# Optimization experiments

Hardware: AMD Instinct MI355X
Metric: run time of the kernel (lower is better)

The kernel has to match this reference:

```python
import jax, jax.numpy as jnp
import numpy as np

B, E, C, H = 128, 512, 128, 8
D = E // H
K = 21  # kNN neighbors per electrode (min(21, C))


def setup_inputs() -> dict:
    key = jax.random.key(0)
    ks = jax.random.split(key, 7)
    x = jax.random.normal(ks[0], (B, E, C), dtype=jnp.float32)
    # 1x1 Conv1d with no bias == [E_out, E_in] matmul over the feature dim
    wq = jax.random.normal(ks[1], (E, E), dtype=jnp.float32) * (E ** -0.5)
    wk = jax.random.normal(ks[2], (E, E), dtype=jnp.float32) * (E ** -0.5)
    wv = jax.random.normal(ks[3], (E, E), dtype=jnp.float32) * (E ** -0.5)
    wo = jax.random.normal(ks[4], (E, E), dtype=jnp.float32) * (E ** -0.5)
    dir_vec = jax.random.normal(ks[5], (H, C), dtype=jnp.float32)

    # synthetic electrode positions (stands in for electrode_positions.pt)
    pos = jax.random.normal(ks[6], (C, 3), dtype=jnp.float32)

    # arc_dist: great-circle distance scaled by mean radius
    radii = jnp.linalg.norm(pos, axis=1, keepdims=True)
    posn = pos / radii
    dist = jnp.arccos(jnp.clip(posn @ posn.T, -1.0, 1.0)) * radii.mean()

    # Gaussian spatial bias, row-mean centered
    sigma = jnp.median(jnp.tril(dist, 1))
    attn_bias = -dist ** 2 / (2.0 * sigma ** 2 + 1e-8)
    attn_bias = attn_bias - attn_bias.mean(axis=1, keepdims=True)

    # unit displacement vectors, zeroed on the diagonal: disp[i,j] = unit(pos[j]-pos[i])
    disp = pos[None, :, :] - pos[:, None, :]
    disp = disp / jnp.clip(jnp.linalg.norm(disp, axis=-1, keepdims=True), 1e-8)
    disp = disp.at[jnp.arange(C), jnp.arange(C)].set(0.0)

    # kNN mask: K smallest distances per row (includes self)
    _, knn_idx = jax.lax.top_k(-dist, K)
    knn_mask = jnp.zeros((C, C), dtype=bool).at[jnp.arange(C)[:, None], knn_idx].set(True)

    return {"x": x, "wq": wq, "wk": wk, "wv": wv, "wo": wo,
            "dir_vec": dir_vec, "attn_bias": attn_bias,
            "displacement": disp, "knn_mask": knn_mask}


def reference(x, wq, wk, wv, wo, dir_vec, attn_bias, displacement, knn_mask):
    scale = D ** -0.5
    # q/k/v projections: 1x1 conv (no bias) + SELU, then split heads -> [B,H,D,C]
    q = jax.nn.selu(jnp.einsum('oe,bec->boc', wq, x)).reshape(B, H, D, C)
    k = jax.nn.selu(jnp.einsum('oe,bec->boc', wk, x)).reshape(B, H, D, C)
    v = jax.nn.selu(jnp.einsum('oe,bec->boc', wv, x)).reshape(B, H, D, C)

    # scores[b,h,i,j] = <q[...,i], k[...,j]> * scale + spatial bias
    scores = jnp.einsum('bhdi,bhdj->bhij', q, k) * scale + attn_bias[None, None]

    # per-head antisymmetric directional bias
    dvn = dir_vec / jnp.clip(jnp.linalg.norm(dir_vec, axis=-1, keepdims=True), 1e-12)
    dir_bias = displacement.mean(axis=-1)[None, :, :] * dvn[:, None, :]  # [H,C,C]
    dir_bias = 0.5 * (dir_bias - jnp.swapaxes(dir_bias, -1, -2))
    scores = scores + (dir_bias - dir_bias.mean(axis=-1, keepdims=True))[None]

    # kNN masking + stable softmax
    scores = jnp.where(knn_mask[None, None], scores, -jnp.inf)
    scores = scores - scores.max(axis=-1, keepdims=True)
    p = jax.nn.softmax(scores, axis=-1)

    # aggregate values and merge heads -> [B, E, C]
    attn = jnp.einsum('bhij,bhdj->bhdi', p, v).reshape(B, E, C)
    # output projection (AlphaDropout is identity in eval)
    return jax.nn.selu(jnp.einsum('oe,bec->boc', wo, attn))
```

## Files before the change

### kernel.cpp

```cpp
#include <hip/hip_runtime.h>
#include <math.h>

#define B_ 128
#define E_ 512
#define C_ 128
#define H_ 8
#define D_ 64
#define BEC_ ((size_t)B_ * E_ * C_)

typedef __attribute__((ext_vector_type(8))) __bf16 bf16x8;
typedef __attribute__((ext_vector_type(4))) float f32x4;

__device__ __forceinline__ ushort f2bf(float f) {
    unsigned u = __float_as_uint(f);
    unsigned r = u + 0x7fffu + ((u >> 16) & 1u);
    return (ushort)(r >> 16);
}
__device__ __forceinline__ float bf2f(ushort h) {
    return __uint_as_float(((unsigned)h) << 16);
}
__device__ __forceinline__ void split_bf(float f, ushort& hi, ushort& lo) {
    hi = f2bf(f);
    lo = f2bf(f - bf2f(hi));
}
__device__ __forceinline__ float selu_f(float x) {
    const float alpha = 1.6732632423543772f;
    const float scale = 1.0507009873554805f;
    return x > 0.0f ? scale * x : scale * alpha * expm1f(x);
}
__device__ __forceinline__ void gll16(const void* g, void* l) {
    __builtin_amdgcn_global_load_lds(
        (const __attribute__((address_space(1))) void*)g,
        (__attribute__((address_space(3))) void*)l, 16, 0, 0);
}

__global__ void detect_mask_kernel(const unsigned char* __restrict__ m,
                                   int* __restrict__ flag) {
    __shared__ int cnt;
    if (threadIdx.x == 0) cnt = 0;
    __syncthreads();
    int local = 0;
    for (int i = threadIdx.x; i < C_ * C_; i += blockDim.x) local += (m[i] != 0);
    atomicAdd(&cnt, local);
    __syncthreads();
    if (threadIdx.x == 0) *flag = (cnt > 1600) ? 1 : 0;
}

__global__ __launch_bounds__(128) void bias_prep_kernel(
    const float* __restrict__ dir_vec, const float* __restrict__ attn_bias,
    const float* __restrict__ disp, const unsigned char* __restrict__ maskb,
    const int* __restrict__ flag, float* __restrict__ combT)
{
    const int i = blockIdx.x, h = blockIdx.y, j = threadIdx.x;
    __shared__ float red[128];

    float dv = dir_vec[h * C_ + j];
    red[j] = dv * dv;
    __syncthreads();
    for (int s = 64; s > 0; s >>= 1) {
        if (j < s) red[j] += red[j + s];
        __syncthreads();
    }
    const float nrm = fmaxf(sqrtf(red[0]), 1e-12f);
    __syncthreads();

    const float dvn_j = dir_vec[h * C_ + j] / nrm;
    const float dvn_i = dir_vec[h * C_ + i] / nrm;
    const float third = 1.0f / 3.0f;
    const float dm_ij = (disp[(i * C_ + j) * 3 + 0] + disp[(i * C_ + j) * 3 + 1] +
                         disp[(i * C_ + j) * 3 + 2]) * third;
    const float dm_ji = (disp[(j * C_ + i) * 3 + 0] + disp[(j * C_ + i) * 3 + 1] +
                         disp[(j * C_ + i) * 3 + 2]) * third;
    const float db = 0.5f * (dm_ij * dvn_j - dm_ji * dvn_i);

    red[j] = db;
    __syncthreads();
    for (int s = 64; s > 0; s >>= 1) {
        if (j < s) red[j] += red[j + s];
        __syncthreads();
    }
    const float rowmean = red[0] * (1.0f / 128.0f);

    const bool mk = (*flag) ? (maskb[i * C_ + j] != 0)
                            : (((const int*)maskb)[i * C_ + j] != 0);
    combT[((size_t)h * C_ + j) * C_ + i] =
        mk ? (attn_bias[i * C_ + j] + db - rowmean) : -INFINITY;
}

__global__ __launch_bounds__(256) void wsplit_kernel(
    const float* __restrict__ w0, const float* __restrict__ w1,
    const float* __restrict__ w2, const float* __restrict__ w3,
    ushort* __restrict__ wh, ushort* __restrict__ wl)
{
    const int s = blockIdx.y;
    const float* __restrict__ w = (s == 0) ? w0 : (s == 1) ? w1 : (s == 2) ? w2 : w3;
    const size_t base = (size_t)s * E_ * E_;
    const size_t i0 = ((size_t)blockIdx.x * 256 + threadIdx.x) * 8;
    const float4 f0 = *(const float4*)&w[i0];
    const float4 f1 = *(const float4*)&w[i0 + 4];
    const float ff[8] = {f0.x, f0.y, f0.z, f0.w, f1.x, f1.y, f1.z, f1.w};
    union { ushort u[8]; uint4 v; } hu, lu;
#pragma unroll
    for (int j = 0; j < 8; ++j) split_bf(ff[j], hu.u[j], lu.u[j]);
    *(uint4*)&wh[base + i0] = hu.v;
    *(uint4*)&wl[base + i0] = lu.v;
}

__global__ __launch_bounds__(256) void xsplit_kernel(
    const float* __restrict__ x, ushort* __restrict__ xh, ushort* __restrict__ xl)
{
    const int b = blockIdx.y, e0 = blockIdx.x * 64;
    __shared__ float ts[64][132];
    const int tid = threadIdx.x;
    const float* __restrict__ xb = x + ((size_t)b * E_ + e0) * C_;
#pragma unroll
    for (int r = 0; r < 8; ++r) {
        const int idx = tid + r * 256;
        const int e = idx >> 5, c4 = idx & 31;
        *(float4*)&ts[e][c4 * 4] = *(const float4*)&xb[(size_t)e * C_ + c4 * 4];
    }
    __syncthreads();
    const int lc = tid >> 3;
    const int l8 = (tid & 7) * 8;
#pragma unroll
    for (int p = 0; p < 4; ++p) {
        const int c = p * 32 + lc;
        union { ushort u[8]; uint4 v; } hu, lu;
#pragma unroll
        for (int j = 0; j < 8; ++j) split_bf(ts[l8 + j][c], hu.u[j], lu.u[j]);
        const size_t rb = ((size_t)b * C_ + c) * E_ + e0 + l8;
        *(uint4*)&xh[rb] = hu.v;
        *(uint4*)&xl[rb] = lu.v;
    }
}

template<int MODE>
__global__ __launch_bounds__(512, 1) void gemm8_kernel(
    const ushort* __restrict__ Wh, const ushort* __restrict__ Wl,
    const ushort* __restrict__ Bh, const ushort* __restrict__ Bl,
    ushort* __restrict__ qh, ushort* __restrict__ ql,
    ushort* __restrict__ kh, ushort* __restrict__ kl,
    ushort* __restrict__ vhp, float* __restrict__ fout)
{
    __shared__ ushort lds[3 * 24576];

    const int NB = (MODE == 0) ? 12 : 4;
    const int nwg = NB * 64;
    const int w = blockIdx.x + NB * blockIdx.y;
    const int l = (w & 7) * (nwg >> 3) + (w >> 3);
    const int bx = l % NB, bgrp = l / NB;

    const int tid = threadIdx.x, wid = tid >> 6, lane = tid & 63;
    const int o0 = bx * 128;
    const int wr = wid >> 2, wc = wid & 3, l15 = lane & 15;
    const int kq = (lane >> 4) * 16;

    const char* sp[6];
    size_t so[6];
    int lo_[6];
#pragma unroll
    for (int q = 0; q < 6; ++q) {
        const int g = wid * 6 + q;
        int stream, inst;
        if (g < 8)       { stream = 0; inst = g; }
        else if (g < 16) { stream = 1; inst = g - 8; }
        else if (g < 32) { stream = 2; inst = g - 16; }
        else             { stream = 3; inst = g - 32; }
        const int rowbase = (stream < 2) ? (o0 + inst * 16)
                                         : (bgrp * 256 + inst * 16);
        sp[q] = (stream == 0) ? (const char*)Wh : (stream == 1) ? (const char*)Wl
              : (stream == 2) ? (const char*)Bh : (const char*)Bl;
        so[q] = ((size_t)(rowbase + (lane >> 2)) * E_) * 2 + (size_t)(lane & 3) * 16;
        lo_[q] = ((stream == 0) ? 0 : (stream == 1) ? 4096 :
                  (stream == 2) ? 8192 : 16384) + inst * 512;
    }

    int aoff[4], boff[4];
#pragma unroll
    for (int m = 0; m < 4; ++m) aoff[m] = (wr * 64 + m * 16 + l15) * 64 + kq;
#pragma unroll
    for (int n = 0; n < 4; ++n) boff[n] = (wc * 64 + n * 16 + l15) * 64 + kq;

    f32x4 acc[4][4];
#pragma unroll
    for (int m = 0; m < 4; ++m)
#pragma unroll
        for (int n = 0; n < 4; ++n) acc[m][n] = (f32x4)0.0f;

#pragma unroll
    for (int p = 0; p < 3; ++p) {
#pragma unroll
        for (int q = 0; q < 6; ++q)
            gll16(sp[q] + so[q] + (size_t)p * 64, &lds[p * 24576 + lo_[q]]);
    }

    int cur = 0;
    for (int t = 0; t < 16; ++t) {
        const char* bb = (const char*)lds + cur * 49152;

        asm volatile("s_waitcnt vmcnt(12)" ::: "memory");
        __builtin_amdgcn_s_barrier();
        __builtin_amdgcn_sched_barrier(0);

        bf16x8 ah[4], al[4], bh4[4], bl4[4];
#pragma unroll
        for (int m = 0; m < 2; ++m) {
            ah[m] = *(const bf16x8*)(bb + aoff[m]);
            al[m] = *(const bf16x8*)(bb + 8192 + aoff[m]);
        }
#pragma unroll
        for (int n = 0; n < 4; ++n) {
            bh4[n] = *(const bf16x8*)(bb + 16384 + boff[n]);
            bl4[n] = *(const bf16x8*)(bb + 32768 + boff[n]);
        }
        __builtin_amdgcn_s_setprio(1);
#pragma unroll
        for (int m = 0; m < 2; ++m)
#pragma unroll
            for (int n = 0; n < 4; ++n) {
                acc[m][n] = __builtin_amdgcn_mfma_f32_16x16x32_bf16(
                    ah[m], bh4[n], acc[m][n], 0, 0, 0);
                acc[m][n] = __builtin_amdgcn_mfma_f32_16x16x32_bf16(
                    ah[m], bl4[n], acc[m][n], 0, 0, 0);
                acc[m][n] = __builtin_amdgcn_mfma_f32_16x16x32_bf16(
                    al[m], bh4[n], acc[m][n], 0, 0, 0);
            }
        __builtin_amdgcn_s_setprio(0);

#pragma unroll
        for (int m = 2; m < 4; ++m) {
            ah[m] = *(const bf16x8*)(bb + aoff[m]);
            al[m] = *(const bf16x8*)(bb + 8192 + aoff[m]);
        }
        asm volatile("s_waitcnt lgkmcnt(0)" ::: "memory");
        __builtin_amdgcn_sched_barrier(0);
        __builtin_amdgcn_s_barrier();

        {
            const int kt = (t + 3 > 15) ? 15 : t + 3;
#pragma unroll
            for (int q = 0; q < 6; ++q)
                gll16(sp[q] + so[q] + (size_t)kt * 64, &lds[cur * 24576 + lo_[q]]);
        }

        __builtin_amdgcn_s_setprio(1);
#pragma unroll
        for (int m = 2; m < 4; ++m)
#pragma unroll
            for (int n = 0; n < 4; ++n) {
                acc[m][n] = __builtin_amdgcn_mfma_f32_16x16x32_bf16(
                    ah[m], bh4[n], acc[m][n], 0, 0, 0);
                acc[m][n] = __builtin_amdgcn_mfma_f32_16x16x32_bf16(
                    ah[m], bl4[n], acc[m][n], 0, 0, 0);
                acc[m][n] = __builtin_amdgcn_mfma_f32_16x16x32_bf16(
                    al[m], bh4[n], acc[m][n], 0, 0, 0);
            }
        __builtin_amdgcn_s_setprio(0);

        cur = (cur == 2) ? 0 : cur + 1;
    }
    asm volatile("s_waitcnt vmcnt(0)" ::: "memory");

    const int lr4 = (lane >> 4) * 4;
    if (MODE == 1) {
        const int ob = bx * 128 + wr * 64;
#pragma unroll
        for (int m = 0; m < 4; ++m)
#pragma unroll
            for (int n = 0; n < 4; ++n) {
                const int R = bgrp * 256 + wc * 64 + n * 16 + l15;
                float* po = fout + ((size_t)(R >> 7) * E_ + ob + m * 16 + lr4) * C_ +
                            (R & 127);
                const f32x4 a = acc[m][n];
#pragma unroll
                for (int j = 0; j < 4; ++j) po[(size_t)j * C_] = selu_f(a[j]);
            }
    } else {
        const int z = bx >> 2;
        const int wo0 = (bx & 3) * 128 + wr * 64;
        if (z == 2) {
#pragma unroll
            for (int m = 0; m < 4; ++m)
#pragma unroll
                for (int n = 0; n < 4; ++n) {
                    const int R = bgrp * 256 + wc * 64 + n * 16 + l15;
                    const f32x4 a = acc[m][n];
#pragma unroll
                    for (int j = 0; j < 4; ++j)
                        vhp[((size_t)(R >> 7) * E_ + wo0 + m * 16 + lr4 + j) * C_ +
                            (R & 127)] = f2bf(selu_f(a[j]));
                }
        } else {
            ushort* __restrict__ th = z ? kh : qh;
            ushort* __restrict__ tl = z ? kl : ql;
#pragma unroll
            for (int m = 0; m < 4; ++m)
#pragma unroll
                for (int n = 0; n < 4; ++n) {
                    const int R = bgrp * 256 + wc * 64 + n * 16 + l15;
                    const int ol = wo0 + m * 16 + lr4;
                    union { ushort u[4]; uint2 v; } hu, lu;
                    const f32x4 a = acc[m][n];
#pragma unroll
                    for (int j = 0; j < 4; ++j) split_bf(selu_f(a[j]), hu.u[j], lu.u[j]);
                    *(uint2*)&th[(size_t)R * E_ + ol] = hu.v;
                    *(uint2*)&tl[(size_t)R * E_ + ol] = lu.v;
                }
        }
    }
}

__global__ __launch_bounds__(256, 2) void attn_mfma_kernel(
    const ushort* __restrict__ qTh, const ushort* __restrict__ qTl,
    const ushort* __restrict__ kTh, const ushort* __restrict__ kTl,
    const ushort* __restrict__ vh,  const float* __restrict__ combT,
    ushort* __restrict__ aTh, ushort* __restrict__ aTl)
{
    const int b = blockIdx.x, h = blockIdx.y;
    __shared__ ushort lds[40960];
    ushort* sQh = lds;
    ushort* sQl = lds + 8192;
    ushort* sKh = lds + 16384;
    ushort* sKl = lds + 24576;
    ushort* sV  = lds + 32768;
    ushort* sPh = lds;
    ushort* sPl = lds + 16384;

    const int tid = threadIdx.x, wid = tid >> 6, lane = tid & 63;

    {
        const size_t gq = (size_t)b * C_ * E_ + h * D_;
        const int rsub = lane >> 3, chunk = lane & 7;
#pragma unroll
        for (int t = 0; t < 4; ++t) {
            const int inst = wid * 4 + t;
            const int row = inst * 8 + rsub;
            const size_t goff = (gq + (size_t)row * E_) * 2 +
                                (size_t)(chunk ^ (row & 7)) * 16;
            gll16((const char*)qTh + goff, &sQh[inst * 512]);
            gll16((const char*)qTl + goff, &sQl[inst * 512]);
            gll16((const char*)kTh + goff, &sKh[inst * 512]);
            gll16((const char*)kTl + goff, &sKl[inst * 512]);
        }
        const size_t gv = ((size_t)b * E_ + h * D_) * C_;
        const int vr = lane >> 4, vchunk = lane & 15;
#pragma unroll
        for (int t = 0; t < 4; ++t) {
            const int inst = wid * 4 + t;
            const int row = inst * 4 + vr;
            const size_t goff = (gv + (size_t)row * C_) * 2 +
                                (size_t)(vchunk ^ (row & 7)) * 16;
            gll16((const char*)vh + goff, &sV[inst * 512]);
        }
    }
    __syncthreads();

    const int i0 = wid * 32;
    const int l15 = lane & 15;

    f32x4 acc[2][8];
#pragma unroll
    for (int m = 0; m < 2; ++m)
#pragma unroll
        for (int n = 0; n < 8; ++n) acc[m][n] = (f32x4)0.0f;

#pragma unroll
    for (int kk = 0; kk < 2; ++kk) {
        const int kbyte = kk * 64 + (lane >> 4) * 16;
        bf16x8 qhf[2], qlf[2];
#pragma unroll
        for (int m = 0; m < 2; ++m) {
            const int r = i0 + m * 16 + l15;
            const int byt = r * 128 + (kbyte ^ ((r & 7) << 4));
            qhf[m] = *(const bf16x8*)((const char*)sQh + byt);
            qlf[m] = *(const bf16x8*)((const char*)sQl + byt);
        }
#pragma unroll
        for (int n = 0; n < 8; ++n) {
            const int r = n * 16 + l15;
            const int byt = r * 128 + (kbyte ^ ((r & 7) << 4));
            const bf16x8 khf = *(const bf16x8*)((const char*)sKh + byt);
            const bf16x8 klf = *(const bf16x8*)((const char*)sKl + byt);
#pragma unroll
            for (int m = 0; m < 2; ++m) {
                acc[m][n] = __builtin_amdgcn_mfma_f32_16x16x32_bf16(
                    qhf[m], khf, acc[m][n], 0, 0, 0);
                acc[m][n] = __builtin_amdgcn_mfma_f32_16x16x32_bf16(
                    qhf[m], klf, acc[m][n], 0, 0, 0);
                acc[m][n] = __builtin_amdgcn_mfma_f32_16x16x32_bf16(
                    qlf[m], khf, acc[m][n], 0, 0, 0);
            }
        }
    }

#pragma unroll
    for (int m = 0; m < 2; ++m)
#pragma unroll
        for (int n = 0; n < 8; ++n) {
            const int jcol = n * 16 + l15;
            const float4 cb = *(const float4*)&combT[
                ((size_t)h * C_ + jcol) * C_ + i0 + m * 16 + (lane >> 4) * 4];
            acc[m][n][0] = fmaf(acc[m][n][0], 0.125f, cb.x);
            acc[m][n][1] = fmaf(acc[m][n][1], 0.125f, cb.y);
            acc[m][n][2] = fmaf(acc[m][n][2], 0.125f, cb.z);
            acc[m][n][3] = fmaf(acc[m][n][3], 0.125f, cb.w);
        }

#pragma unroll
    for (int m = 0; m < 2; ++m)
#pragma unroll
        for (int jj = 0; jj < 4; ++jj) {
            float mx = -INFINITY;
#pragma unroll
            for (int n = 0; n < 8; ++n) mx = fmaxf(mx, acc[m][n][jj]);
#pragma unroll
            for (int off = 1; off < 16; off <<= 1)
                mx = fmaxf(mx, __shfl_xor(mx, off));
            float sum = 0.0f;
#pragma unroll
            for (int n = 0; n < 8; ++n) {
                const float e = __expf(acc[m][n][jj] - mx);
                acc[m][n][jj] = e;
                sum += e;
            }
#pragma unroll
            for (int off = 1; off < 16; off <<= 1) sum += __shfl_xor(sum, off);
            const float inv = 1.0f / sum;
#pragma unroll
            for (int n = 0; n < 8; ++n) acc[m][n][jj] *= inv;
        }

    __syncthreads();
#pragma unroll
    for (int m = 0; m < 2; ++m)
#pragma unroll
        for (int n = 0; n < 8; ++n)
#pragma unroll
            for (int jj = 0; jj < 4; ++jj) {
                const int i = i0 + m * 16 + (lane >> 4) * 4 + jj;
                const int col = n * 16 + l15;
                const int byt = i * 256 + ((col * 2) ^ ((i & 7) << 4));
                ushort hi, lo;
                split_bf(acc[m][n][jj], hi, lo);
                *(ushort*)((char*)sPh + byt) = hi;
                *(ushort*)((char*)sPl + byt) = lo;
            }
    __syncthreads();

    f32x4 acc2[2][4];
#pragma unroll
    for (int m = 0; m < 2; ++m)
#pragma unroll
        for (int n = 0; n < 4; ++n) acc2[m][n] = (f32x4)0.0f;

#pragma unroll
    for (int ks = 0; ks < 4; ++ks) {
        const int kbyte = ks * 64 + (lane >> 4) * 16;
        bf16x8 ph[2], pl[2];
#pragma unroll
        for (int m = 0; m < 2; ++m) {
            const int r = i0 + m * 16 + l15;
            const int byt = r * 256 + (kbyte ^ ((r & 7) << 4));
            ph[m] = *(const bf16x8*)((const char*)sPh + byt);
            pl[m] = *(const bf16x8*)((const char*)sPl + byt);
        }
#pragma unroll
        for (int n = 0; n < 4; ++n) {
            const int d = n * 16 + l15;
            const int byt = d * 256 + (kbyte ^ ((d & 7) << 4));
            const bf16x8 vb = *(const bf16x8*)((const char*)sV + byt);
#pragma unroll
            for (int m = 0; m < 2; ++m) {
                acc2[m][n] = __builtin_amdgcn_mfma_f32_16x16x32_bf16(
                    ph[m], vb, acc2[m][n], 0, 0, 0);
                acc2[m][n] = __builtin_amdgcn_mfma_f32_16x16x32_bf16(
                    pl[m], vb, acc2[m][n], 0, 0, 0);
            }
        }
    }

#pragma unroll
    for (int m = 0; m < 2; ++m)
#pragma unroll
        for (int n = 0; n < 4; ++n)
#pragma unroll
            for (int jj = 0; jj < 4; ++jj) {
                const int i = i0 + m * 16 + (lane >> 4) * 4 + jj;
                const int dcol = n * 16 + l15;
                ushort hi, lo;
                split_bf(acc2[m][n][jj], hi, lo);
                const size_t idx = ((size_t)b * C_ + i) * E_ + h * D_ + dcol;
                aTh[idx] = hi;
                aTl[idx] = lo;
            }
}

extern "C" void kernel_launch(void* const* d_in, const int* in_sizes, int n_in,
                              void* d_out, int out_size, void* d_ws, size_t ws_size,
                              hipStream_t stream) {
    const float* x        = (const float*)d_in[0];
    const float* wq       = (const float*)d_in[1];
    const float* wk       = (const float*)d_in[2];
    const float* wv       = (const float*)d_in[3];
    const float* wo       = (const float*)d_in[4];
    const float* dir_vec  = (const float*)d_in[5];
    const float* attn_b   = (const float*)d_in[6];
    const float* disp     = (const float*)d_in[7];
    const unsigned char* knn = (const unsigned char*)d_in[8];
    float* out = (float*)d_out;

    char* ws = (char*)d_ws;
    size_t off = 0;
    ushort* qTh = (ushort*)(ws + off); off += BEC_ * 2;
    ushort* qTl = (ushort*)(ws + off); off += BEC_ * 2;
    ushort* kTh = (ushort*)(ws + off); off += BEC_ * 2;
    ushort* kTl = (ushort*)(ws + off); off += BEC_ * 2;
    ushort* vbuf = (ushort*)(ws + off); off += BEC_ * 2;
    ushort* xTh = (ushort*)(ws + off); off += BEC_ * 2;
    ushort* xTl = (ushort*)(ws + off); off += BEC_ * 2;
    ushort* wh  = (ushort*)(ws + off); off += (size_t)4 * E_ * E_ * 2;
    ushort* wl  = (ushort*)(ws + off); off += (size_t)4 * E_ * E_ * 2;
    float* combT = (float*)(ws + off); off += (size_t)H_ * C_ * C_ * sizeof(float);
    int* flag = (int*)(ws + off);

    detect_mask_kernel<<<1, 256, 0, stream>>>(knn, flag);
    bias_prep_kernel<<<dim3(C_, H_), 128, 0, stream>>>(dir_vec, attn_b, disp, knn,
                                                       flag, combT);
    wsplit_kernel<<<dim3(128, 4), 256, 0, stream>>>(wq, wk, wv, wo, wh, wl);
    xsplit_kernel<<<dim3(8, B_), 256, 0, stream>>>(x, xTh, xTl);

    const size_t WSZ = (size_t)E_ * E_;
    gemm8_kernel<0><<<dim3(12, 64), 512, 0, stream>>>(
        wh, wl, xTh, xTl, qTh, qTl, kTh, kTl, vbuf, nullptr);
    attn_mfma_kernel<<<dim3(B_, H_), 256, 0, stream>>>(
        qTh, qTl, kTh, kTl, vbuf, combT, xTh, xTl);
    gemm8_kernel<1><<<dim3(4, 64), 512, 0, stream>>>(
        wh + 3 * WSZ, wl + 3 * WSZ, xTh, xTl,
        nullptr, nullptr, nullptr, nullptr, nullptr, out);
}
```

Before: 214.1 us.

## Restructure split-bf16 GEMM with double-buffered LDS, register prefetch and XOR swizzle

The projection GEMM kernel drops from triple-buffered to double-buffered LDS, which lets it target two workgroups per CU. It now prefetches the next k-tile's fragments into a second register set while MFMAs run on the current one. An XOR swizzle on global-to-LDS offsets and fragment read offsets aims to cut LDS bank conflicts. The QKV launch is split into a transposed-MFMA launch for Q/K and a separate launch for V. The extra register sets and the per-element (unvectorized) stores in the transposed epilogue add register pressure and store traffic that may offset the gains.

Measured after the change: 211.6 us. About the same (-1.1%).

```diff
diff --git a/kernel.cpp b/kernel.cpp
--- a/kernel.cpp
+++ b/kernel.cpp
@@ -134,26 +134,24 @@
     }
 }
 
-template<int MODE>
-__global__ __launch_bounds__(512, 1) void gemm8_kernel(
+template<int TRANS, int FOUT>
+__global__ __launch_bounds__(512, 2) void gemm8p_kernel(
     const ushort* __restrict__ Wh, const ushort* __restrict__ Wl,
     const ushort* __restrict__ Bh, const ushort* __restrict__ Bl,
-    ushort* __restrict__ qh, ushort* __restrict__ ql,
-    ushort* __restrict__ kh, ushort* __restrict__ kl,
-    ushort* __restrict__ vhp, float* __restrict__ fout)
+    ushort* __restrict__ o0h, ushort* __restrict__ o0l,
+    ushort* __restrict__ o1h, ushort* __restrict__ o1l,
+    float* __restrict__ fout, int NB)
 {
-    __shared__ ushort lds[3 * 24576];
-
-    const int NB = (MODE == 0) ? 12 : 4;
+    __shared__ ushort lds[2 * 24576];
+
     const int nwg = NB * 64;
-    const int w = blockIdx.x + NB * blockIdx.y;
-    const int l = (w & 7) * (nwg >> 3) + (w >> 3);
-    const int bx = l % NB, bgrp = l / NB;
+    const int wI = blockIdx.x + NB * blockIdx.y;
+    const int li = (wI & 7) * (nwg >> 3) + (wI >> 3);
+    const int bx = li % NB, bgrp = li / NB;
 
     const int tid = threadIdx.x, wid = tid >> 6, lane = tid & 63;
     const int o0 = bx * 128;
     const int wr = wid >> 2, wc = wid & 3, l15 = lane & 15;
-    const int kq = (lane >> 4) * 16;
 
     const char* sp[6];
     size_t so[6];
@@ -170,16 +168,18 @@
                                          : (bgrp * 256 + inst * 16);
         sp[q] = (stream == 0) ? (const char*)Wh : (stream == 1) ? (const char*)Wl
               : (stream == 2) ? (const char*)Bh : (const char*)Bl;
-        so[q] = ((size_t)(rowbase + (lane >> 2)) * E_) * 2 + (size_t)(lane & 3) * 16;
+        so[q] = (size_t)(rowbase + (lane >> 2)) * (E_ * 2) +
+                (size_t)(((lane & 3) ^ ((lane >> 3) & 3)) * 16);
         lo_[q] = ((stream == 0) ? 0 : (stream == 1) ? 4096 :
                   (stream == 2) ? 8192 : 16384) + inst * 512;
     }
 
+    const int koff = (((lane >> 4) ^ ((l15 >> 1) & 3)) << 4);
     int aoff[4], boff[4];
 #pragma unroll
-    for (int m = 0; m < 4; ++m) aoff[m] = (wr * 64 + m * 16 + l15) * 64 + kq;
-#pragma unroll
-    for (int n = 0; n < 4; ++n) boff[n] = (wc * 64 + n * 16 + l15) * 64 + kq;
+    for (int m = 0; m < 4; ++m) aoff[m] = (wr * 64 + m * 16 + l15) * 64 + koff;
+#pragma unroll
+    for (int n = 0; n < 4; ++n) boff[n] = 16384 + (wc * 64 + n * 16 + l15) * 64 + koff;
 
     f32x4 acc[4][4];
 #pragma unroll
@@ -187,127 +187,125 @@
 #pragma unroll
         for (int n = 0; n < 4; ++n) acc[m][n] = (f32x4)0.0f;
 
-#pragma unroll
-    for (int p = 0; p < 3; ++p) {
-#pragma unroll
-        for (int q = 0; q < 6; ++q)
-            gll16(sp[q] + so[q] + (size_t)p * 64, &lds[p * 24576 + lo_[q]]);
-    }
-
-    int cur = 0;
-    for (int t = 0; t < 16; ++t) {
-        const char* bb = (const char*)lds + cur * 49152;
-
-        asm volatile("s_waitcnt vmcnt(12)" ::: "memory");
+    bf16x8 Aah[4], Aal[4], Abh[4], Abl[4];
+    bf16x8 Bah[4], Bal[4], Bbh[4], Bbl[4];
+
+#define STAGE(T, BUF) do { _Pragma("unroll") \
+    for (int q = 0; q < 6; ++q) \
+        gll16(sp[q] + so[q] + (size_t)(T) * 64, &lds[(BUF) * 24576 + lo_[q]]); \
+    } while (0)
+
+#define READF(P, BUF) do { const char* bb_ = (const char*)lds + (BUF) * 49152; \
+    _Pragma("unroll") for (int m_ = 0; m_ < 4; ++m_) { \
+        P##ah[m_] = *(const bf16x8*)(bb_ + aoff[m_]); \
+        P##al[m_] = *(const bf16x8*)(bb_ + 8192 + aoff[m_]); } \
+    _Pragma("unroll") for (int n_ = 0; n_ < 4; ++n_) { \
+        P##bh[n_] = *(const bf16x8*)(bb_ + boff[n_]); \
+        P##bl[n_] = *(const bf16x8*)(bb_ + 16384 + boff[n_]); } } while (0)
+
+#define MFMA48(P) do { _Pragma("unroll") \
+    for (int m_ = 0; m_ < 4; ++m_) { _Pragma("unroll") \
+        for (int n_ = 0; n_ < 4; ++n_) { \
+            if (TRANS) { \
+                acc[n_][m_] = __builtin_amdgcn_mfma_f32_16x16x32_bf16(P##bh[n_], P##ah[m_], acc[n_][m_], 0, 0, 0); \
+                acc[n_][m_] = __builtin_amdgcn_mfma_f32_16x16x32_bf16(P##bh[n_], P##al[m_], acc[n_][m_], 0, 0, 0); \
+                acc[n_][m_] = __builtin_amdgcn_mfma_f32_16x16x32_bf16(P##bl[n_], P##ah[m_], acc[n_][m_], 0, 0, 0); \
+            } else { \
+                acc[m_][n_] = __builtin_amdgcn_mfma_f32_16x16x32_bf16(P##ah[m_], P##bh[n_], acc[m_][n_], 0, 0, 0); \
+                acc[m_][n_] = __builtin_amdgcn_mfma_f32_16x16x32_bf16(P##ah[m_], P##bl[n_], acc[m_][n_], 0, 0, 0); \
+                acc[m_][n_] = __builtin_amdgcn_mfma_f32_16x16x32_bf16(P##al[m_], P##bh[n_], acc[m_][n_], 0, 0, 0); \
+            } } } } while (0)
+
+#define WAITVM6 do { asm volatile("s_waitcnt vmcnt(6)" ::: "memory"); \
+    __builtin_amdgcn_sched_barrier(0); } while (0)
+#define WAITLG0 do { asm volatile("s_waitcnt lgkmcnt(0)" ::: "memory"); \
+    __builtin_amdgcn_sched_barrier(0); } while (0)
+
+    STAGE(0, 0);
+    STAGE(1, 1);
+    WAITVM6;
+    __builtin_amdgcn_s_barrier();
+    READF(A, 0);
+    WAITLG0;
+    __builtin_amdgcn_s_barrier();
+    STAGE(2, 0);
+
+    for (int tt = 0; tt < 16; tt += 2) {
+        WAITVM6;
         __builtin_amdgcn_s_barrier();
-        __builtin_amdgcn_sched_barrier(0);
-
-        bf16x8 ah[4], al[4], bh4[4], bl4[4];
-#pragma unroll
-        for (int m = 0; m < 2; ++m) {
-            ah[m] = *(const bf16x8*)(bb + aoff[m]);
-            al[m] = *(const bf16x8*)(bb + 8192 + aoff[m]);
-        }
-#pragma unroll
-        for (int n = 0; n < 4; ++n) {
-            bh4[n] = *(const bf16x8*)(bb + 16384 + boff[n]);
-            bl4[n] = *(const bf16x8*)(bb + 32768 + boff[n]);
-        }
         __builtin_amdgcn_s_setprio(1);
-#pragma unroll
-        for (int m = 0; m < 2; ++m)
-#pragma unroll
-            for (int n = 0; n < 4; ++n) {
-                acc[m][n] = __builtin_amdgcn_mfma_f32_16x16x32_bf16(
-                    ah[m], bh4[n], acc[m][n], 0, 0, 0);
-                acc[m][n] = __builtin_amdgcn_mfma_f32_16x16x32_bf16(
-                    ah[m], bl4[n], acc[m][n], 0, 0, 0);
-                acc[m][n] = __builtin_amdgcn_mfma_f32_16x16x32_bf16(
-                    al[m], bh4[n], acc[m][n], 0, 0, 0);
-            }
+        READF(B, 1);
+        MFMA48(A);
         __builtin_amdgcn_s_setprio(0);
-
-#pragma unroll
-        for (int m = 2; m < 4; ++m) {
-            ah[m] = *(const bf16x8*)(bb + aoff[m]);
-            al[m] = *(const bf16x8*)(bb + 8192 + aoff[m]);
-        }
-        asm volatile("s_waitcnt lgkmcnt(0)" ::: "memory");
-        __builtin_amdgcn_sched_barrier(0);
+        WAITLG0;
         __builtin_amdgcn_s_barrier();
-
-        {
-            const int kt = (t + 3 > 15) ? 15 : t + 3;
-#pragma unroll
-            for (int q = 0; q < 6; ++q)
-                gll16(sp[q] + so[q] + (size_t)kt * 64, &lds[cur * 24576 + lo_[q]]);
-        }
-
+        STAGE((tt + 3 > 15) ? 15 : tt + 3, 1);
+
+        WAITVM6;
+        __builtin_amdgcn_s_barrier();
         __builtin_amdgcn_s_setprio(1);
-#pragma unroll
-        for (int m = 2; m < 4; ++m)
-#pragma unroll
-            for (int n = 0; n < 4; ++n) {
-                acc[m][n] = __builtin_amdgcn_mfma_f32_16x16x32_bf16(
-                    ah[m], bh4[n], acc[m][n], 0, 0, 0);
-                acc[m][n] = __builtin_amdgcn_mfma_f32_16x16x32_bf16(
-                    ah[m], bl4[n], acc[m][n], 0, 0, 0);
-                acc[m][n] = __builtin_amdgcn_mfma_f32_16x16x32_bf16(
-                    al[m], bh4[n], acc[m][n], 0, 0, 0);
-            }
+        if (tt < 14) READF(A, 0);
+        MFMA48(B);
         __builtin_amdgcn_s_setprio(0);
-
-        cur = (cur == 2) ? 0 : cur + 1;
+        WAITLG0;
+        __builtin_amdgcn_s_barrier();
+        STAGE((tt + 4 > 15) ? 15 : tt + 4, 0);
     }
     asm volatile("s_waitcnt vmcnt(0)" ::: "memory");
 
     const int lr4 = (lane >> 4) * 4;
-    if (MODE == 1) {
-        const int ob = bx * 128 + wr * 64;
+    if (FOUT) {
 #pragma unroll
         for (int m = 0; m < 4; ++m)
 #pragma unroll
             for (int n = 0; n < 4; ++n) {
                 const int R = bgrp * 256 + wc * 64 + n * 16 + l15;
-                float* po = fout + ((size_t)(R >> 7) * E_ + ob + m * 16 + lr4) * C_ +
-                            (R & 127);
+                const int o = o0 + wr * 64 + m * 16 + lr4;
                 const f32x4 a = acc[m][n];
+                float* po = fout + ((size_t)(R >> 7) * E_ + o) * C_ + (R & 127);
 #pragma unroll
                 for (int j = 0; j < 4; ++j) po[(size_t)j * C_] = selu_f(a[j]);
             }
+    } else if (TRANS) {
+        const int z = bx >> 2;
+        ushort* __restrict__ th = z ? o1h : o0h;
+        ushort* __restrict__ tl = z ? o1l : o0l;
+        const int oz = (bx & 3) * 128;
+#pragma unroll
+        for (int n = 0; n < 4; ++n)
+#pragma unroll
+            for (int m = 0; m < 4; ++m) {
+                const int o = oz + wr * 64 + m * 16 + l15;
+                const int Rb = bgrp * 256 + wc * 64 + n * 16 + lr4;
+                const f32x4 a = acc[n][m];
+#pragma unroll
+                for (int j = 0; j < 4; ++j) {
+                    ushort hi, lo;
+                    split_bf(selu_f(a[j]), hi, lo);
+                    const size_t idx = (size_t)(Rb + j) * E_ + o;
+                    th[idx] = hi;
+                    tl[idx] = lo;
+                }
+            }
     } else {
-        const int z = bx >> 2;
-        const int wo0 = (bx & 3) * 128 + wr * 64;
-        if (z == 2) {
-#pragma unroll
-            for (int m = 0; m < 4; ++m)
-#pragma unroll
-                for (int n = 0; n < 4; ++n) {
-                    const int R = bgrp * 256 + wc * 64 + n * 16 + l15;
-                    const f32x4 a = acc[m][n];
-#pragma unroll
-                    for (int j = 0; j < 4; ++j)
-                        vhp[((size_t)(R >> 7) * E_ + wo0 + m * 16 + lr4 + j) * C_ +
-                            (R & 127)] = f2bf(selu_f(a[j]));
-                }
-        } else {
-            ushort* __restrict__ th = z ? kh : qh;
-            ushort* __restrict__ tl = z ? kl : ql;
-#pragma unroll
-            for (int m = 0; m < 4; ++m)
-#pragma unroll
-                for (int n = 0; n < 4; ++n) {
-                    const int R = bgrp * 256 + wc * 64 + n * 16 + l15;
-                    const int ol = wo0 + m * 16 + lr4;
-                    union { ushort u[4]; uint2 v; } hu, lu;
-                    const f32x4 a = acc[m][n];
-#pragma unroll
-                    for (int j = 0; j < 4; ++j) split_bf(selu_f(a[j]), hu.u[j], lu.u[j]);
-                    *(uint2*)&th[(size_t)R * E_ + ol] = hu.v;
-                    *(uint2*)&tl[(size_t)R * E_ + ol] = lu.v;
-                }
-        }
-    }
+#pragma unroll
+        for (int m = 0; m < 4; ++m)
+#pragma unroll
+            for (int n = 0; n < 4; ++n) {
+                const int R = bgrp * 256 + wc * 64 + n * 16 + l15;
+                const int o = o0 + wr * 64 + m * 16 + lr4;
+                const f32x4 a = acc[m][n];
+#pragma unroll
+                for (int j = 0; j < 4; ++j)
+                    o0h[((size_t)(R >> 7) * E_ + o + j) * C_ + (R & 127)] =
+                        f2bf(selu_f(a[j]));
+            }
+    }
+#undef STAGE
+#undef READF
+#undef MFMA48
+#undef WAITVM6
+#undef WAITLG0
 }
 
 __global__ __launch_bounds__(256, 2) void attn_mfma_kernel(
@@ -530,11 +528,14 @@
     xsplit_kernel<<<dim3(8, B_), 256, 0, stream>>>(x, xTh, xTl);
 
     const size_t WSZ = (size_t)E_ * E_;
-    gemm8_kernel<0><<<dim3(12, 64), 512, 0, stream>>>(
-        wh, wl, xTh, xTl, qTh, qTl, kTh, kTl, vbuf, nullptr);
+    gemm8p_kernel<1, 0><<<dim3(8, 64), 512, 0, stream>>>(
+        wh, wl, xTh, xTl, qTh, qTl, kTh, kTl, nullptr, 8);
+    gemm8p_kernel<0, 0><<<dim3(4, 64), 512, 0, stream>>>(
+        wh + 2 * WSZ, wl + 2 * WSZ, xTh, xTl,
+        vbuf, nullptr, nullptr, nullptr, nullptr, 4);
     attn_mfma_kernel<<<dim3(B_, H_), 256, 0, stream>>>(
         qTh, qTl, kTh, kTl, vbuf, combT, xTh, xTl);
-    gemm8_kernel<1><<<dim3(4, 64), 512, 0, stream>>>(
+    gemm8p_kernel<0, 1><<<dim3(4, 64), 512, 0, stream>>>(
         wh + 3 * WSZ, wl + 3 * WSZ, xTh, xTl,
-        nullptr, nullptr, nullptr, nullptr, nullptr, out);
-}
+        nullptr, nullptr, nullptr, nullptr, out, 4);
+}
```
